# Performance work log

Measured on AMD Instinct MI355X. Metric: run time of the kernel, lower is better.

## Reference

```python
import jax, jax.numpy as jnp
import numpy as np

# 6 pairwise combinations of the 4 ray coordinates (decomp='2d')
COMBS = np.array([[0, 1], [0, 2], [0, 3], [1, 2], [1, 3], [2, 3]])
RAY_MIN = 0.0
RAY_MAX = 1.0
N_RAYS = 262144
GRID_DIM = 16
MLP_DIM = GRID_DIM * 6 * 3  # grid_dim * n_combs * n_levels = 288
MLP_WIDTH = 128


def _bilinear(grid_c, pts):
    """grid_c: [C,H,W] feature plane; pts: [N,2] in [0,1].
    Bilinear interpolation with align_corners=True semantics (grid_sample)."""
    C, H, W = grid_c.shape
    u = pts[:, 0] * (H - 1)
    v = pts[:, 1] * (W - 1)
    u0 = jnp.clip(jnp.floor(u), 0, H - 2).astype(jnp.int32)
    v0 = jnp.clip(jnp.floor(v), 0, W - 2).astype(jnp.int32)
    u1 = u0 + 1
    v1 = v0 + 1
    wu = (u - u0.astype(u.dtype))[None, :]  # [1,N]
    wv = (v - v0.astype(v.dtype))[None, :]
    g00 = grid_c[:, u0, v0]  # [C,N]
    g01 = grid_c[:, u0, v1]
    g10 = grid_c[:, u1, v0]
    g11 = grid_c[:, u1, v1]
    out = (g00 * (1 - wu) * (1 - wv) + g01 * (1 - wu) * wv
           + g10 * wu * (1 - wv) + g11 * wu * wv)
    return out.T  # [N,C]


def _level_feats(grids, coords):
    """grids: [6,C,H,W]; coords: [N,6,2] -> [N, 6*C] (comb-minor order)."""
    f = jax.vmap(_bilinear, in_axes=(0, 1))(grids, coords)  # [6,N,C]
    n = coords.shape[0]
    return jnp.moveaxis(f, 0, 1).reshape(n, -1)


def setup_inputs() -> dict:
    key = jax.random.key(0)
    ks = jax.random.split(key, 8)
    ray = jax.random.uniform(ks[0], (N_RAYS, 4), dtype=jnp.float32)
    grids_l0 = jax.random.normal(ks[1], (6, GRID_DIM, 128, 128), dtype=jnp.float32) * 0.1
    grids_l1 = jax.random.normal(ks[2], (6, GRID_DIM, 256, 256), dtype=jnp.float32) * 0.1
    grids_l2 = jax.random.normal(ks[3], (6, GRID_DIM, 512, 512), dtype=jnp.float32) * 0.1
    w1 = jax.random.normal(ks[4], (MLP_DIM, MLP_WIDTH), dtype=jnp.float32) * (1.0 / np.sqrt(MLP_DIM))
    b1 = jnp.zeros((MLP_WIDTH,), dtype=jnp.float32)
    w2 = jax.random.normal(ks[5], (MLP_WIDTH, 3), dtype=jnp.float32) * (1.0 / np.sqrt(MLP_WIDTH))
    b2 = jnp.zeros((3,), dtype=jnp.float32)
    return {"ray": ray, "grids_l0": grids_l0, "grids_l1": grids_l1,
            "grids_l2": grids_l2, "w1": w1, "b1": b1, "w2": w2, "b2": b2}


def reference(ray, grids_l0, grids_l1, grids_l2, w1, b1, w2, b2):
    # normalize rays into [0,1] using ray_min/ray_max buffers
    pts = (ray - RAY_MIN) / (RAY_MAX - RAY_MIN)
    coords = pts[:, COMBS]  # [N,6,2]
    # level-major, combination-minor concat (matches the nested forward loops)
    feats = jnp.concatenate(
        [_level_feats(g, coords) for g in (grids_l0, grids_l1, grids_l2)], axis=-1)
    h = jax.nn.relu(feats @ w1 + b1)
    return jax.nn.sigmoid(h @ w2 + b2)
```

## Files before the change

### kernel.cpp

```cpp
#include <hip/hip_runtime.h>
#include <hip/hip_bf16.h>
#include <cstdint>
#include <cstddef>

#define N_RAYS 262144
#define NR 32
#define THREADS 256
#define FSTRIDE 292

#define T0_OFF 0u
#define T1_OFF 1572864u
#define T2_OFF 7864320u
#define T_ELEMS 33030144u
#define FEAT_BYTE_OFF 66060288u
#define FEAT_DWORDS 37748736u
#define W1F_BYTE_OFF 217055232u
#define W1F_BYTES 73728u
#define KEYS_OFF   217128960u
#define PERM_OFF   217653248u
#define HIST_OFF   218701824u
#define OFFS_OFF   218963968u
#define RSORT_OFF  219226112u
#define NEED_SORT  223420416u

typedef __attribute__((ext_vector_type(8))) short short8v;
typedef __attribute__((ext_vector_type(4))) float float4v;

__device__ __forceinline__ float bf_lo(uint32_t w) { return __uint_as_float(w << 16); }
__device__ __forceinline__ float bf_hi(uint32_t w) { return __uint_as_float(w & 0xFFFF0000u); }

__device__ __forceinline__ float bf_extract(const uint4& q, int i) {
    uint32_t w = ((const uint32_t*)&q)[i >> 1];
    uint32_t h = (i & 1) ? (w & 0xFFFF0000u) : (w << 16);
    return __uint_as_float(h);
}

__device__ __forceinline__ uint16_t f2bf_rne(float f) {
    uint32_t x = __float_as_uint(f);
    uint32_t r = x + 0x7FFFu + ((x >> 16) & 1u);
    return (uint16_t)(r >> 16);
}

__device__ __forceinline__ float sel4(const float4& p, int i) {
    float r = p.x;
    r = (i == 1) ? p.y : r;
    r = (i == 2) ? p.z : r;
    r = (i == 3) ? p.w : r;
    return r;
}

__device__ __forceinline__ uint32_t morton4(const float4& p) {
    int q0 = min(15, max(0, (int)(p.x * 16.0f)));
    int q1 = min(15, max(0, (int)(p.y * 16.0f)));
    int q2 = min(15, max(0, (int)(p.z * 16.0f)));
    int q3 = min(15, max(0, (int)(p.w * 16.0f)));
    uint32_t key = 0;
    #pragma unroll
    for (int b = 0; b < 4; ++b) {
        key |= (uint32_t)((q0 >> b) & 1) << (4 * b + 0);
        key |= (uint32_t)((q1 >> b) & 1) << (4 * b + 1);
        key |= (uint32_t)((q2 >> b) & 1) << (4 * b + 2);
        key |= (uint32_t)((q3 >> b) & 1) << (4 * b + 3);
    }
    return key;
}

__global__ void transpose_kernel(const float* __restrict__ in,
                                 __hip_bfloat16* __restrict__ out, int H) {
    int idx = blockIdx.x * blockDim.x + threadIdx.x;
    int hh = H * H;
    int total = 6 * hh;
    if (idx >= total) return;
    int c = idx / hh;
    int rem = idx - c * hh;
    const float* ip = in + (size_t)c * 16 * hh + rem;
    uint32_t words[8];
    #pragma unroll
    for (int j = 0; j < 8; ++j) {
        uint16_t lo = f2bf_rne(ip[(size_t)(2 * j) * hh]);
        uint16_t hi = f2bf_rne(ip[(size_t)(2 * j + 1) * hh]);
        words[j] = (uint32_t)lo | ((uint32_t)hi << 16);
    }
    uint4* op = (uint4*)((uint16_t*)out + (size_t)idx * 16);
    op[0] = make_uint4(words[0], words[1], words[2], words[3]);
    op[1] = make_uint4(words[4], words[5], words[6], words[7]);
}

__global__ void w1_pack_kernel(const float* __restrict__ w1, uint16_t* __restrict__ w1f) {
    int t = blockIdx.x * 64 + threadIdx.x;
    if (t >= 8 * 9 * 64) return;
    int lane = t & 63;
    int fr = t >> 6;
    int ct = fr / 9;
    int kc = fr - ct * 9;
    int col = ct * 16 + (lane & 15);
    int krow = kc * 32 + (lane >> 4) * 8;
    uint32_t od[4];
    #pragma unroll
    for (int j = 0; j < 4; ++j) {
        uint16_t lo = f2bf_rne(w1[(size_t)(krow + 2 * j) * 128 + col]);
        uint16_t hi = f2bf_rne(w1[(size_t)(krow + 2 * j + 1) * 128 + col]);
        od[j] = (uint32_t)lo | ((uint32_t)hi << 16);
    }
    *(uint4*)(w1f + (size_t)t * 8) = make_uint4(od[0], od[1], od[2], od[3]);
}

__global__ void key_hist_kernel(const float4* __restrict__ ray,
                                uint16_t* __restrict__ keys,
                                uint32_t* __restrict__ hist) {
    int r = blockIdx.x * 256 + threadIdx.x;
    float4 p = ray[r];
    uint32_t key = morton4(p);
    keys[r] = (uint16_t)key;
    atomicAdd(&hist[key], 1u);
}

__global__ void scanA_kernel(const uint32_t* __restrict__ hist, uint32_t* __restrict__ bsum) {
    __shared__ uint32_t s[256];
    int t = threadIdx.x;
    s[t] = hist[blockIdx.x * 256 + t];
    __syncthreads();
    for (int d = 128; d > 0; d >>= 1) {
        if (t < d) s[t] += s[t + d];
        __syncthreads();
    }
    if (t == 0) bsum[blockIdx.x] = s[0];
}

__global__ void scanB_kernel(uint32_t* __restrict__ bsum) {
    __shared__ uint32_t s[256];
    int t = threadIdx.x;
    uint32_t v = bsum[t];
    s[t] = v;
    __syncthreads();
    for (int d = 1; d < 256; d <<= 1) {
        uint32_t x = (t >= d) ? s[t - d] : 0;
        __syncthreads();
        s[t] += x;
        __syncthreads();
    }
    bsum[t] = s[t] - v;
}

__global__ void scanC_kernel(const uint32_t* __restrict__ hist,
                             const uint32_t* __restrict__ bsum,
                             uint32_t* __restrict__ offs) {
    __shared__ uint32_t s[256];
    int t = threadIdx.x, b = blockIdx.x;
    uint32_t v = hist[b * 256 + t];
    s[t] = v;
    __syncthreads();
    for (int d = 1; d < 256; d <<= 1) {
        uint32_t x = (t >= d) ? s[t - d] : 0;
        __syncthreads();
        s[t] += x;
        __syncthreads();
    }
    offs[b * 256 + t] = bsum[b] + s[t] - v;
}

__global__ void scatter_kernel(const float4* __restrict__ ray,
                               const uint16_t* __restrict__ keys,
                               uint32_t* __restrict__ offs,
                               uint32_t* __restrict__ perm,
                               float4* __restrict__ ray_sorted) {
    int r = blockIdx.x * 256 + threadIdx.x;
    uint32_t key = keys[r];
    uint32_t pos = atomicAdd(&offs[key], 1u);
    perm[pos] = (uint32_t)r;
    ray_sorted[pos] = ray[r];
}

__global__ __launch_bounds__(256, 4) void fused_gmlp_kernel(
    const float4* __restrict__ rsort, const uint16_t* __restrict__ gt,
    const uint16_t* __restrict__ w1f, const float* __restrict__ bias1,
    const float* __restrict__ w2, const float* __restrict__ bias2,
    const uint32_t* __restrict__ perm, float* __restrict__ out) {
    __shared__ uint32_t s_feats[32 * 148];
    __shared__ float s_w2[384];
    __shared__ float4 s_ray[32];

    int tid = threadIdx.x;
    int wvid = tid >> 6;
    int lane = tid & 63;
    int swz = ((blockIdx.x & 7) << 10) + (blockIdx.x >> 3);
    int r0 = swz << 5;

    if (tid < 32) s_ray[tid] = rsort[r0 + tid];
    s_w2[tid] = w2[tid];
    if (tid < 128) s_w2[256 + tid] = w2[256 + tid];
    __syncthreads();

    for (int s = wvid; s < 9; s += 4) {
        int interp = 2 * s + (lane >> 5);
        int r = lane & 31;
        int level = (interp >= 12) ? 2 : ((interp >= 6) ? 1 : 0);
        int comb = interp - level * 6;
        int H = 128 << level;
        float4 p = s_ray[r];
        int c0 = (0x211000 >> (4 * comb)) & 0xF;
        int c1 = (0x332321 >> (4 * comb)) & 0xF;
        float u = sel4(p, c0) * (float)(H - 1);
        float v = sel4(p, c1) * (float)(H - 1);
        float u0f = fminf(fmaxf(floorf(u), 0.0f), (float)(H - 2));
        float v0f = fminf(fmaxf(floorf(v), 0.0f), (float)(H - 2));
        float fu = u - u0f, fv = v - v0f;
        int u0 = (int)u0f, v0 = (int)v0f;

        uint32_t lvl_off = (level == 0) ? T0_OFF : ((level == 1) ? T1_OFF : T2_OFF);
        const uint16_t* gp0 = gt + lvl_off + (((size_t)comb * H + u0) * H + v0) * 16;
        const uint4* q0 = (const uint4*)gp0;
        const uint4* q1 = (const uint4*)(gp0 + (size_t)16 * H);
        uint4 a0 = q0[0], a1 = q0[1], a2 = q0[2], a3 = q0[3];
        uint4 b0 = q1[0], b1 = q1[1], b2 = q1[2], b3 = q1[3];

        uint32_t c00[8], c01[8], c10[8], c11[8];
        #pragma unroll
        for (int j = 0; j < 4; ++j) {
            c00[j] = ((const uint32_t*)&a0)[j];  c00[j + 4] = ((const uint32_t*)&a1)[j];
            c01[j] = ((const uint32_t*)&a2)[j];  c01[j + 4] = ((const uint32_t*)&a3)[j];
            c10[j] = ((const uint32_t*)&b0)[j];  c10[j + 4] = ((const uint32_t*)&b1)[j];
            c11[j] = ((const uint32_t*)&b2)[j];  c11[j + 4] = ((const uint32_t*)&b3)[j];
        }

        float w00 = (1.0f - fu) * (1.0f - fv);
        float w01 = (1.0f - fu) * fv;
        float w10 = fu * (1.0f - fv);
        float w11 = fu * fv;

        uint32_t od[8];
        #pragma unroll
        for (int j = 0; j < 8; ++j) {
            float lo = w00 * bf_lo(c00[j]) + w01 * bf_lo(c01[j]) +
                       w10 * bf_lo(c10[j]) + w11 * bf_lo(c11[j]);
            float hi = w00 * bf_hi(c00[j]) + w01 * bf_hi(c01[j]) +
                       w10 * bf_hi(c10[j]) + w11 * bf_hi(c11[j]);
            od[j] = (uint32_t)f2bf_rne(lo) | ((uint32_t)f2bf_rne(hi) << 16);
        }
        uint32_t* op = &s_feats[r * 148 + interp * 8];
        *(uint4*)op       = make_uint4(od[0], od[1], od[2], od[3]);
        *(uint4*)(op + 4) = make_uint4(od[4], od[5], od[6], od[7]);
    }
    __syncthreads();

    float b1c0 = bias1[wvid * 32 + (lane & 15)];
    float b1c1 = bias1[wvid * 32 + 16 + (lane & 15)];
    int lg = lane >> 4;
    const uint32_t* arow = &s_feats[(lane & 15) * 148 + lg * 4];

    float4v acc00, acc10, acc01, acc11;
    {
        short8v bfrA[9];
        #pragma unroll
        for (int kc = 0; kc < 9; ++kc)
            bfrA[kc] = *(const short8v*)(w1f + (((size_t)((wvid * 2) * 9 + kc)) * 64 + lane) * 8);
        #pragma unroll
        for (int j = 0; j < 4; ++j) { acc00[j] = b1c0; acc10[j] = b1c0; }
        #pragma unroll
        for (int kc = 0; kc < 9; ++kc) {
            short8v a0 = *(const short8v*)(arow + kc * 16);
            short8v a1 = *(const short8v*)(arow + 16 * 148 + kc * 16);
            acc00 = __builtin_amdgcn_mfma_f32_16x16x32_bf16(a0, bfrA[kc], acc00, 0, 0, 0);
            acc10 = __builtin_amdgcn_mfma_f32_16x16x32_bf16(a1, bfrA[kc], acc10, 0, 0, 0);
        }
    }
    {
        short8v bfrB[9];
        #pragma unroll
        for (int kc = 0; kc < 9; ++kc)
            bfrB[kc] = *(const short8v*)(w1f + (((size_t)((wvid * 2 + 1) * 9 + kc)) * 64 + lane) * 8);
        #pragma unroll
        for (int j = 0; j < 4; ++j) { acc01[j] = b1c1; acc11[j] = b1c1; }
        #pragma unroll
        for (int kc = 0; kc < 9; ++kc) {
            short8v a0 = *(const short8v*)(arow + kc * 16);
            short8v a1 = *(const short8v*)(arow + 16 * 148 + kc * 16);
            acc01 = __builtin_amdgcn_mfma_f32_16x16x32_bf16(a0, bfrB[kc], acc01, 0, 0, 0);
            acc11 = __builtin_amdgcn_mfma_f32_16x16x32_bf16(a1, bfrB[kc], acc11, 0, 0, 0);
        }
    }
    __syncthreads();

    float* s_h = (float*)s_feats;
    {
        int c0 = wvid * 32 + (lane & 15);
        int rb = lg * 4;
        #pragma unroll
        for (int j = 0; j < 4; ++j) {
            s_h[(rb + j) * 132 + c0]            = fmaxf(acc00[j], 0.0f);
            s_h[(rb + j) * 132 + c0 + 16]       = fmaxf(acc01[j], 0.0f);
            s_h[(rb + j + 16) * 132 + c0]       = fmaxf(acc10[j], 0.0f);
            s_h[(rb + j + 16) * 132 + c0 + 16]  = fmaxf(acc11[j], 0.0f);
        }
    }
    __syncthreads();

    int ray = tid >> 3;
    int jg = tid & 7;
    int j0 = jg * 16;
    float p0 = 0.f, p1 = 0.f, p2 = 0.f;
    #pragma unroll
    for (int qq = 0; qq < 4; ++qq) {
        float4 hv = *(const float4*)&s_h[ray * 132 + j0 + qq * 4];
        const float* w2a = &s_w2[(j0 + qq * 4) * 3];
        p0 += hv.x * w2a[0] + hv.y * w2a[3] + hv.z * w2a[6] + hv.w * w2a[9];
        p1 += hv.x * w2a[1] + hv.y * w2a[4] + hv.z * w2a[7] + hv.w * w2a[10];
        p2 += hv.x * w2a[2] + hv.y * w2a[5] + hv.z * w2a[8] + hv.w * w2a[11];
    }
    p0 += __shfl_xor(p0, 1); p0 += __shfl_xor(p0, 2); p0 += __shfl_xor(p0, 4);
    p1 += __shfl_xor(p1, 1); p1 += __shfl_xor(p1, 2); p1 += __shfl_xor(p1, 4);
    p2 += __shfl_xor(p2, 1); p2 += __shfl_xor(p2, 2); p2 += __shfl_xor(p2, 4);

    if (jg == 0) {
        int orig = (int)perm[r0 + ray];
        float o0 = 1.0f / (1.0f + expf(-(p0 + bias2[0])));
        float o1 = 1.0f / (1.0f + expf(-(p1 + bias2[1])));
        float o2 = 1.0f / (1.0f + expf(-(p2 + bias2[2])));
        float* op = out + (size_t)orig * 3;
        op[0] = o0; op[1] = o1; op[2] = o2;
    }
}

__global__ __launch_bounds__(256, 8) void gather_t_kernel(
    const float4* __restrict__ ray, const uint16_t* __restrict__ gt,
    uint32_t* __restrict__ featsT) {
    int lb = (blockIdx.x & 7) * 2304 + (blockIdx.x >> 3);
    int interp = lb >> 10;
    int r = ((lb & 1023) << 8) + threadIdx.x;
    int level = interp / 6;
    int comb = interp - level * 6;
    int H = 128 << level;

    float4 p = ray[r];
    int c0 = (0x211000 >> (4 * comb)) & 0xF;
    int c1 = (0x332321 >> (4 * comb)) & 0xF;
    float u = sel4(p, c0) * (float)(H - 1);
    float v = sel4(p, c1) * (float)(H - 1);
    float u0f = fminf(fmaxf(floorf(u), 0.0f), (float)(H - 2));
    float v0f = fminf(fmaxf(floorf(v), 0.0f), (float)(H - 2));
    float wu = u - u0f, wv = v - v0f;
    int u0 = (int)u0f, v0 = (int)v0f;

    uint32_t lvl_off = (level == 0) ? T0_OFF : ((level == 1) ? T1_OFF : T2_OFF);
    const uint16_t* gp0 = gt + lvl_off + (((size_t)comb * H + u0) * H + v0) * 16;
    const uint4* q0 = (const uint4*)gp0;
    const uint4* q1 = (const uint4*)(gp0 + (size_t)16 * H);
    uint4 a0 = q0[0], a1 = q0[1], a2 = q0[2], a3 = q0[3];
    uint4 b0 = q1[0], b1 = q1[1], b2 = q1[2], b3 = q1[3];

    uint32_t c00[8], c01[8], c10[8], c11[8];
    #pragma unroll
    for (int j = 0; j < 4; ++j) {
        c00[j] = ((const uint32_t*)&a0)[j];  c00[j + 4] = ((const uint32_t*)&a1)[j];
        c01[j] = ((const uint32_t*)&a2)[j];  c01[j + 4] = ((const uint32_t*)&a3)[j];
        c10[j] = ((const uint32_t*)&b0)[j];  c10[j + 4] = ((const uint32_t*)&b1)[j];
        c11[j] = ((const uint32_t*)&b2)[j];  c11[j + 4] = ((const uint32_t*)&b3)[j];
    }

    float w00 = (1.0f - wu) * (1.0f - wv);
    float w01 = (1.0f - wu) * wv;
    float w10 = wu * (1.0f - wv);
    float w11 = wu * wv;

    uint32_t od[8];
    #pragma unroll
    for (int j = 0; j < 8; ++j) {
        float lo = w00 * bf_lo(c00[j]) + w01 * bf_lo(c01[j]) +
                   w10 * bf_lo(c10[j]) + w11 * bf_lo(c11[j]);
        float hi = w00 * bf_hi(c00[j]) + w01 * bf_hi(c01[j]) +
                   w10 * bf_hi(c10[j]) + w11 * bf_hi(c11[j]);
        od[j] = (uint32_t)f2bf_rne(lo) | ((uint32_t)f2bf_rne(hi) << 16);
    }

    uint4* op = (uint4*)(featsT + ((size_t)interp * N_RAYS + r) * 8);
    op[0] = make_uint4(od[0], od[1], od[2], od[3]);
    op[1] = make_uint4(od[4], od[5], od[6], od[7]);
}

__global__ __launch_bounds__(256, 2) void mfma_mlp_kernel(
    const uint16_t* __restrict__ featsT,
    const uint16_t* __restrict__ w1f,
    const float* __restrict__ bias1,
    const float* __restrict__ w2, const float* __restrict__ bias2,
    const uint32_t* __restrict__ perm,
    float* __restrict__ out, int tiles_per_block) {
    __shared__ float s_h[32][132];

    int tid = threadIdx.x;
    int wv = tid >> 6;
    int lane = tid & 63;

    short8v bfr[2][9];
    #pragma unroll
    for (int ctl = 0; ctl < 2; ++ctl) {
        int ct = wv * 2 + ctl;
        #pragma unroll
        for (int kc = 0; kc < 9; ++kc)
            bfr[ctl][kc] = *(const short8v*)(w1f + (((size_t)(ct * 9 + kc)) * 64 + lane) * 8);
    }
    float b1c0 = bias1[wv * 32 + (lane & 15)];
    float b1c1 = bias1[wv * 32 + 16 + (lane & 15)];

    int jg = tid & 7;
    int j0 = jg * 16;
    float w2r0[16], w2r1[16], w2r2[16];
    #pragma unroll
    for (int jj = 0; jj < 16; ++jj) {
        const float* w2p = w2 + (size_t)(j0 + jj) * 3;
        w2r0[jj] = w2p[0]; w2r1[jj] = w2p[1]; w2r2[jj] = w2p[2];
    }
    float bb0 = bias2[0], bb1 = bias2[1], bb2 = bias2[2];

    int lg = lane >> 4;
    int half8 = (lg & 1) * 8;
    int ipo = lg >> 1;

    for (int it = 0; it < tiles_per_block; ++it) {
        int tile = blockIdx.x * tiles_per_block + it;
        int r0 = tile * 32;
        int rA = r0 + (lane & 15);

        short8v af[18];
        #pragma unroll
        for (int kc = 0; kc < 9; ++kc) {
            size_t base = ((size_t)(2 * kc + ipo) * N_RAYS + rA) * 16 + half8;
            af[kc]     = *(const short8v*)(featsT + base);
            af[9 + kc] = *(const short8v*)(featsT + base + 256);
        }

        float4v acc00, acc01, acc10, acc11;
        #pragma unroll
        for (int j = 0; j < 4; ++j) { acc00[j] = b1c0; acc01[j] = b1c1; acc10[j] = b1c0; acc11[j] = b1c1; }

        #pragma unroll
        for (int kc = 0; kc < 9; ++kc) {
            acc00 = __builtin_amdgcn_mfma_f32_16x16x32_bf16(af[kc],     bfr[0][kc], acc00, 0, 0, 0);
            acc01 = __builtin_amdgcn_mfma_f32_16x16x32_bf16(af[kc],     bfr[1][kc], acc01, 0, 0, 0);
            acc10 = __builtin_amdgcn_mfma_f32_16x16x32_bf16(af[9 + kc], bfr[0][kc], acc10, 0, 0, 0);
            acc11 = __builtin_amdgcn_mfma_f32_16x16x32_bf16(af[9 + kc], bfr[1][kc], acc11, 0, 0, 0);
        }

        __syncthreads();
        {
            int c0 = wv * 32 + (lane & 15);
            int rb = (lane >> 4) * 4;
            #pragma unroll
            for (int j = 0; j < 4; ++j) {
                s_h[rb + j][c0]           = fmaxf(acc00[j], 0.0f);
                s_h[rb + j][c0 + 16]      = fmaxf(acc01[j], 0.0f);
                s_h[rb + j + 16][c0]      = fmaxf(acc10[j], 0.0f);
                s_h[rb + j + 16][c0 + 16] = fmaxf(acc11[j], 0.0f);
            }
        }
        __syncthreads();

        int ray = tid >> 3;
        float p0 = 0.f, p1 = 0.f, p2 = 0.f;
        #pragma unroll
        for (int qq = 0; qq < 4; ++qq) {
            float4 hv = *(const float4*)&s_h[ray][j0 + qq * 4];
            float h0 = hv.x, h1 = hv.y, h2 = hv.z, h3 = hv.w;
            p0 += h0 * w2r0[qq * 4] + h1 * w2r0[qq * 4 + 1] + h2 * w2r0[qq * 4 + 2] + h3 * w2r0[qq * 4 + 3];
            p1 += h0 * w2r1[qq * 4] + h1 * w2r1[qq * 4 + 1] + h2 * w2r1[qq * 4 + 2] + h3 * w2r1[qq * 4 + 3];
            p2 += h0 * w2r2[qq * 4] + h1 * w2r2[qq * 4 + 1] + h2 * w2r2[qq * 4 + 2] + h3 * w2r2[qq * 4 + 3];
        }
        p0 += __shfl_xor(p0, 1); p0 += __shfl_xor(p0, 2); p0 += __shfl_xor(p0, 4);
        p1 += __shfl_xor(p1, 1); p1 += __shfl_xor(p1, 2); p1 += __shfl_xor(p1, 4);
        p2 += __shfl_xor(p2, 1); p2 += __shfl_xor(p2, 2); p2 += __shfl_xor(p2, 4);

        if (jg == 0) {
            int orig = perm ? (int)perm[r0 + ray] : (r0 + ray);
            float o0 = 1.0f / (1.0f + expf(-(p0 + bb0)));
            float o1 = 1.0f / (1.0f + expf(-(p1 + bb1)));
            float o2 = 1.0f / (1.0f + expf(-(p2 + bb2)));
            float* op = out + (size_t)orig * 3;
            op[0] = o0; op[1] = o1; op[2] = o2;
        }
    }
}

template <bool USE_T>
__global__ __launch_bounds__(THREADS) void fused_kernel(
    const float4* __restrict__ ray,
    const float* __restrict__ g0, const float* __restrict__ g1,
    const float* __restrict__ g2,
    const __hip_bfloat16* __restrict__ gt,
    const float* __restrict__ weights1, const float* __restrict__ bias1,
    const float* __restrict__ weights2, const float* __restrict__ bias2,
    float* __restrict__ out) {
    __shared__ float4 s_ray[NR];
    __shared__ float s_feats[NR][FSTRIDE];

    int tid = threadIdx.x;
    int rbase = blockIdx.x * NR;
    if (tid < NR) s_ray[tid] = ray[rbase + tid];
    __syncthreads();

    for (int t = tid; t < NR * 36; t += THREADS) {
        int r = t / 36;
        int rem = t - r * 36;
        int interp = rem >> 1;
        int half = rem & 1;
        int level = (interp >= 12) ? 2 : ((interp >= 6) ? 1 : 0);
        int comb = interp - level * 6;
        int H = 128 << level;
        float4 p = s_ray[r];
        int c0 = (0x211000 >> (4 * comb)) & 0xF;
        int c1 = (0x332321 >> (4 * comb)) & 0xF;
        float u = sel4(p, c0) * (float)(H - 1);
        float v = sel4(p, c1) * (float)(H - 1);
        float u0f = fminf(fmaxf(floorf(u), 0.0f), (float)(H - 2));
        float v0f = fminf(fmaxf(floorf(v), 0.0f), (float)(H - 2));
        float wu = u - u0f, wv = v - v0f;
        int u0 = (int)u0f, v0 = (int)v0f;
        float w00 = (1.0f - wu) * (1.0f - wv);
        float w01 = (1.0f - wu) * wv;
        float w10 = wu * (1.0f - wv);
        float w11 = wu * wv;
        float f[8];
        if (USE_T) {
            uint32_t lvl_off = (level == 0) ? T0_OFF : ((level == 1) ? T1_OFF : T2_OFF);
            const uint16_t* gp = (const uint16_t*)gt + lvl_off +
                                 (((size_t)comb * H + u0) * H + v0) * 16 + half * 8;
            uint4 a00 = *(const uint4*)gp;
            uint4 a01 = *(const uint4*)(gp + 16);
            uint4 a10 = *(const uint4*)(gp + (size_t)16 * H);
            uint4 a11 = *(const uint4*)(gp + (size_t)16 * H + 16);
            #pragma unroll
            for (int i = 0; i < 8; ++i) {
                f[i] = w00 * bf_extract(a00, i) + w01 * bf_extract(a01, i) +
                       w10 * bf_extract(a10, i) + w11 * bf_extract(a11, i);
            }
        } else {
            const float* gp = (level == 0) ? g0 : ((level == 1) ? g1 : g2);
            const float* base = gp + ((size_t)(comb * 16 + half * 8) * H + u0) * H + v0;
            #pragma unroll
            for (int i = 0; i < 8; ++i) {
                const float* q = base + (size_t)i * H * H;
                float a00 = q[0], a01 = q[1], a10 = q[H], a11 = q[H + 1];
                f[i] = w00 * a00 + w01 * a01 + w10 * a10 + w11 * a11;
            }
        }
        int fo = interp * 16 + half * 8;
        float* fp = &s_feats[r][fo];
        #pragma unroll
        for (int i = 0; i < 8; ++i) fp[i] = f[i];
    }
    __syncthreads();

    int r = tid >> 3;
    int jg = tid & 7;
    int j0 = jg * 16;
    float acc[16];
    #pragma unroll
    for (int jj = 0; jj < 16; ++jj) acc[jj] = bias1[j0 + jj];

    const float* wp = weights1 + j0;
    for (int k = 0; k < 288; k += 4) {
        float4 fv = *(const float4*)&s_feats[r][k];
        #pragma unroll
        for (int kk = 0; kk < 4; ++kk) {
            const float4* wr = (const float4*)(wp + (size_t)(k + kk) * 128);
            float fk = (kk == 0) ? fv.x : ((kk == 1) ? fv.y : ((kk == 2) ? fv.z : fv.w));
            float4 wa = wr[0], wb = wr[1], wc = wr[2], wd = wr[3];
            acc[0]  += fk * wa.x; acc[1]  += fk * wa.y; acc[2]  += fk * wa.z; acc[3]  += fk * wa.w;
            acc[4]  += fk * wb.x; acc[5]  += fk * wb.y; acc[6]  += fk * wb.z; acc[7]  += fk * wb.w;
            acc[8]  += fk * wc.x; acc[9]  += fk * wc.y; acc[10] += fk * wc.z; acc[11] += fk * wc.w;
            acc[12] += fk * wd.x; acc[13] += fk * wd.y; acc[14] += fk * wd.z; acc[15] += fk * wd.w;
        }
    }

    float p0 = 0.f, p1 = 0.f, p2 = 0.f;
    #pragma unroll
    for (int jj = 0; jj < 16; ++jj) {
        float h = fmaxf(acc[jj], 0.0f);
        const float* w2r = weights2 + (size_t)(j0 + jj) * 3;
        p0 += h * w2r[0];
        p1 += h * w2r[1];
        p2 += h * w2r[2];
    }
    p0 += __shfl_xor(p0, 1); p0 += __shfl_xor(p0, 2); p0 += __shfl_xor(p0, 4);
    p1 += __shfl_xor(p1, 1); p1 += __shfl_xor(p1, 2); p1 += __shfl_xor(p1, 4);
    p2 += __shfl_xor(p2, 1); p2 += __shfl_xor(p2, 2); p2 += __shfl_xor(p2, 4);

    if (jg == 0) {
        float o0 = 1.0f / (1.0f + expf(-(p0 + bias2[0])));
        float o1 = 1.0f / (1.0f + expf(-(p1 + bias2[1])));
        float o2 = 1.0f / (1.0f + expf(-(p2 + bias2[2])));
        float* op = out + (size_t)(rbase + r) * 3;
        op[0] = o0; op[1] = o1; op[2] = o2;
    }
}

extern "C" void kernel_launch(void* const* d_in, const int* in_sizes, int n_in,
                              void* d_out, int out_size, void* d_ws, size_t ws_size,
                              hipStream_t stream) {
    const float4* ray = (const float4*)d_in[0];
    const float* g0 = (const float*)d_in[1];
    const float* g1 = (const float*)d_in[2];
    const float* g2 = (const float*)d_in[3];
    const float* w1 = (const float*)d_in[4];
    const float* b1 = (const float*)d_in[5];
    const float* w2 = (const float*)d_in[6];
    const float* b2 = (const float*)d_in[7];
    float* out = (float*)d_out;

    const size_t T_BYTES = (size_t)T_ELEMS * 2;
    const size_t NEED = (size_t)W1F_BYTE_OFF + W1F_BYTES;

    if (ws_size >= (size_t)NEED_SORT) {
        char* ws = (char*)d_ws;
        __hip_bfloat16* wsb = (__hip_bfloat16*)d_ws;
        uint32_t* bsum  = (uint32_t*)(ws + FEAT_BYTE_OFF);
        uint16_t* w1f  = (uint16_t*)(ws + W1F_BYTE_OFF);
        uint16_t* keys = (uint16_t*)(ws + KEYS_OFF);
        uint32_t* perm = (uint32_t*)(ws + PERM_OFF);
        uint32_t* hist = (uint32_t*)(ws + HIST_OFF);
        uint32_t* offs = (uint32_t*)(ws + OFFS_OFF);
        float4* rsort  = (float4*)(ws + RSORT_OFF);

        hipMemsetAsync(hist, 0, 65536 * 4, stream);
        transpose_kernel<<<(6 * 128 * 128 + 255) / 256, 256, 0, stream>>>(g0, wsb + T0_OFF, 128);
        transpose_kernel<<<(6 * 256 * 256 + 255) / 256, 256, 0, stream>>>(g1, wsb + T1_OFF, 256);
        transpose_kernel<<<(6 * 512 * 512 + 255) / 256, 256, 0, stream>>>(g2, wsb + T2_OFF, 512);
        w1_pack_kernel<<<72, 64, 0, stream>>>(w1, w1f);
        key_hist_kernel<<<N_RAYS / 256, 256, 0, stream>>>(ray, keys, hist);
        scanA_kernel<<<256, 256, 0, stream>>>(hist, bsum);
        scanB_kernel<<<1, 256, 0, stream>>>(bsum);
        scanC_kernel<<<256, 256, 0, stream>>>(hist, bsum, offs);
        scatter_kernel<<<N_RAYS / 256, 256, 0, stream>>>(ray, keys, offs, perm, rsort);
        fused_gmlp_kernel<<<N_RAYS / 32, 256, 0, stream>>>(
            rsort, (const uint16_t*)wsb, w1f, b1, w2, b2, perm, out);
    } else if (ws_size >= NEED) {
        __hip_bfloat16* wsb = (__hip_bfloat16*)d_ws;
        transpose_kernel<<<(6 * 128 * 128 + 255) / 256, 256, 0, stream>>>(g0, wsb + T0_OFF, 128);
        transpose_kernel<<<(6 * 256 * 256 + 255) / 256, 256, 0, stream>>>(g1, wsb + T1_OFF, 256);
        transpose_kernel<<<(6 * 512 * 512 + 255) / 256, 256, 0, stream>>>(g2, wsb + T2_OFF, 512);
        uint32_t* feats = (uint32_t*)((char*)d_ws + FEAT_BYTE_OFF);
        uint16_t* w1f = (uint16_t*)((char*)d_ws + W1F_BYTE_OFF);
        w1_pack_kernel<<<72, 64, 0, stream>>>(w1, w1f);
        gather_t_kernel<<<18432, 256, 0, stream>>>(ray, (const uint16_t*)wsb, feats);
        const int TILES_PER_BLOCK = 4;
        int nblk = N_RAYS / 32 / TILES_PER_BLOCK;
        mfma_mlp_kernel<<<nblk, 256, 0, stream>>>(
            (const uint16_t*)feats, w1f, b1, w2, b2, nullptr, out, TILES_PER_BLOCK);
    } else if (ws_size >= T_BYTES) {
        __hip_bfloat16* wsb = (__hip_bfloat16*)d_ws;
        transpose_kernel<<<(6 * 128 * 128 + 255) / 256, 256, 0, stream>>>(g0, wsb + T0_OFF, 128);
        transpose_kernel<<<(6 * 256 * 256 + 255) / 256, 256, 0, stream>>>(g1, wsb + T1_OFF, 256);
        transpose_kernel<<<(6 * 512 * 512 + 255) / 256, 256, 0, stream>>>(g2, wsb + T2_OFF, 512);
        fused_kernel<true><<<N_RAYS / NR, THREADS, 0, stream>>>(
            ray, g0, g1, g2, wsb, w1, b1, w2, b2, out);
    } else {
        fused_kernel<false><<<N_RAYS / NR, THREADS, 0, stream>>>(
            ray, g0, g1, g2, nullptr, w1, b1, w2, b2, out);
    }
}
```

Baseline: 196.3 us.

## Merge preprocessing kernels into one launch and raise fused kernel occupancy bound

Folds the three grid transposes, the W1 packing and the Morton key histogram into one prep kernel that dispatches work by block index, replacing five launches with one. This removes per-launch gaps and the tail serialisation between small kernels. It also raises the fused gather+MLP kernel's launch-bounds minimum from 4 to 7 blocks per CU, which pushes the compiler to use fewer registers and may cause spills.

```diff
diff --git a/kernel.cpp b/kernel.cpp
--- a/kernel.cpp
+++ b/kernel.cpp
@@ -23,6 +23,12 @@
 #define RSORT_OFF  219226112u
 #define NEED_SORT  223420416u
 
+#define PB_L0   384
+#define PB_L1   1920
+#define PB_L2   8064
+#define PB_PK   8082
+#define PB_HI   9106
+
 typedef __attribute__((ext_vector_type(8))) short short8v;
 typedef __attribute__((ext_vector_type(4))) float float4v;
 
@@ -65,12 +71,10 @@
     return key;
 }
 
-__global__ void transpose_kernel(const float* __restrict__ in,
-                                 __hip_bfloat16* __restrict__ out, int H) {
-    int idx = blockIdx.x * blockDim.x + threadIdx.x;
+__device__ __forceinline__ void transpose_body(const float* __restrict__ in,
+                                               uint16_t* __restrict__ out,
+                                               int H, int idx) {
     int hh = H * H;
-    int total = 6 * hh;
-    if (idx >= total) return;
     int c = idx / hh;
     int rem = idx - c * hh;
     const float* ip = in + (size_t)c * 16 * hh + rem;
@@ -81,38 +85,48 @@
         uint16_t hi = f2bf_rne(ip[(size_t)(2 * j + 1) * hh]);
         words[j] = (uint32_t)lo | ((uint32_t)hi << 16);
     }
-    uint4* op = (uint4*)((uint16_t*)out + (size_t)idx * 16);
+    uint4* op = (uint4*)(out + (size_t)idx * 16);
     op[0] = make_uint4(words[0], words[1], words[2], words[3]);
     op[1] = make_uint4(words[4], words[5], words[6], words[7]);
 }
 
-__global__ void w1_pack_kernel(const float* __restrict__ w1, uint16_t* __restrict__ w1f) {
-    int t = blockIdx.x * 64 + threadIdx.x;
-    if (t >= 8 * 9 * 64) return;
-    int lane = t & 63;
-    int fr = t >> 6;
-    int ct = fr / 9;
-    int kc = fr - ct * 9;
-    int col = ct * 16 + (lane & 15);
-    int krow = kc * 32 + (lane >> 4) * 8;
-    uint32_t od[4];
-    #pragma unroll
-    for (int j = 0; j < 4; ++j) {
-        uint16_t lo = f2bf_rne(w1[(size_t)(krow + 2 * j) * 128 + col]);
-        uint16_t hi = f2bf_rne(w1[(size_t)(krow + 2 * j + 1) * 128 + col]);
-        od[j] = (uint32_t)lo | ((uint32_t)hi << 16);
-    }
-    *(uint4*)(w1f + (size_t)t * 8) = make_uint4(od[0], od[1], od[2], od[3]);
-}
-
-__global__ void key_hist_kernel(const float4* __restrict__ ray,
-                                uint16_t* __restrict__ keys,
-                                uint32_t* __restrict__ hist) {
-    int r = blockIdx.x * 256 + threadIdx.x;
-    float4 p = ray[r];
-    uint32_t key = morton4(p);
-    keys[r] = (uint16_t)key;
-    atomicAdd(&hist[key], 1u);
+__global__ __launch_bounds__(256) void prep_kernel(
+    const float* __restrict__ g0, const float* __restrict__ g1,
+    const float* __restrict__ g2, const float* __restrict__ w1,
+    const float4* __restrict__ ray,
+    uint16_t* __restrict__ gt, uint16_t* __restrict__ w1f,
+    uint16_t* __restrict__ keys, uint32_t* __restrict__ hist) {
+    int b = blockIdx.x;
+    int tid = threadIdx.x;
+    if (b < PB_L0) {
+        transpose_body(g0, gt + T0_OFF, 128, b * 256 + tid);
+    } else if (b < PB_L1) {
+        transpose_body(g1, gt + T1_OFF, 256, (b - PB_L0) * 256 + tid);
+    } else if (b < PB_L2) {
+        transpose_body(g2, gt + T2_OFF, 512, (b - PB_L1) * 256 + tid);
+    } else if (b < PB_PK) {
+        int t = (b - PB_L2) * 256 + tid;
+        int lane = t & 63;
+        int fr = t >> 6;
+        int ct = fr / 9;
+        int kc = fr - ct * 9;
+        int col = ct * 16 + (lane & 15);
+        int krow = kc * 32 + (lane >> 4) * 8;
+        uint32_t od[4];
+        #pragma unroll
+        for (int j = 0; j < 4; ++j) {
+            uint16_t lo = f2bf_rne(w1[(size_t)(krow + 2 * j) * 128 + col]);
+            uint16_t hi = f2bf_rne(w1[(size_t)(krow + 2 * j + 1) * 128 + col]);
+            od[j] = (uint32_t)lo | ((uint32_t)hi << 16);
+        }
+        *(uint4*)(w1f + (size_t)t * 8) = make_uint4(od[0], od[1], od[2], od[3]);
+    } else {
+        int r = (b - PB_PK) * 256 + tid;
+        float4 p = ray[r];
+        uint32_t key = morton4(p);
+        keys[r] = (uint16_t)key;
+        atomicAdd(&hist[key], 1u);
+    }
 }
 
 __global__ void scanA_kernel(const uint32_t* __restrict__ hist, uint32_t* __restrict__ bsum) {
@@ -171,7 +185,7 @@
     ray_sorted[pos] = ray[r];
 }
 
-__global__ __launch_bounds__(256, 4) void fused_gmlp_kernel(
+__global__ __launch_bounds__(256, 7) void fused_gmlp_kernel(
     const float4* __restrict__ rsort, const uint16_t* __restrict__ gt,
     const uint16_t* __restrict__ w1f, const float* __restrict__ bias1,
     const float* __restrict__ w2, const float* __restrict__ bias2,
@@ -319,6 +333,32 @@
         float* op = out + (size_t)orig * 3;
         op[0] = o0; op[1] = o1; op[2] = o2;
     }
+}
+
+__global__ void transpose_kernel(const float* __restrict__ in,
+                                 __hip_bfloat16* __restrict__ out, int H) {
+    int idx = blockIdx.x * blockDim.x + threadIdx.x;
+    if (idx >= 6 * H * H) return;
+    transpose_body(in, (uint16_t*)out, H, idx);
+}
+
+__global__ void w1_pack_kernel(const float* __restrict__ w1, uint16_t* __restrict__ w1f) {
+    int t = blockIdx.x * 64 + threadIdx.x;
+    if (t >= 8 * 9 * 64) return;
+    int lane = t & 63;
+    int fr = t >> 6;
+    int ct = fr / 9;
+    int kc = fr - ct * 9;
+    int col = ct * 16 + (lane & 15);
+    int krow = kc * 32 + (lane >> 4) * 8;
+    uint32_t od[4];
+    #pragma unroll
+    for (int j = 0; j < 4; ++j) {
+        uint16_t lo = f2bf_rne(w1[(size_t)(krow + 2 * j) * 128 + col]);
+        uint16_t hi = f2bf_rne(w1[(size_t)(krow + 2 * j + 1) * 128 + col]);
+        od[j] = (uint32_t)lo | ((uint32_t)hi << 16);
+    }
+    *(uint4*)(w1f + (size_t)t * 8) = make_uint4(od[0], od[1], od[2], od[3]);
 }
 
 __global__ __launch_bounds__(256, 8) void gather_t_kernel(
@@ -620,11 +660,8 @@
         float4* rsort  = (float4*)(ws + RSORT_OFF);
 
         hipMemsetAsync(hist, 0, 65536 * 4, stream);
-        transpose_kernel<<<(6 * 128 * 128 + 255) / 256, 256, 0, stream>>>(g0, wsb + T0_OFF, 128);
-        transpose_kernel<<<(6 * 256 * 256 + 255) / 256, 256, 0, stream>>>(g1, wsb + T1_OFF, 256);
-        transpose_kernel<<<(6 * 512 * 512 + 255) / 256, 256, 0, stream>>>(g2, wsb + T2_OFF, 512);
-        w1_pack_kernel<<<72, 64, 0, stream>>>(w1, w1f);
-        key_hist_kernel<<<N_RAYS / 256, 256, 0, stream>>>(ray, keys, hist);
+        prep_kernel<<<PB_HI, 256, 0, stream>>>(
+            g0, g1, g2, w1, ray, (uint16_t*)wsb, w1f, keys, hist);
         scanA_kernel<<<256, 256, 0, stream>>>(hist, bsum);
         scanB_kernel<<<1, 256, 0, stream>>>(bsum);
         scanC_kernel<<<256, 256, 0, stream>>>(hist, bsum, offs);
```

New measurement: 194.5 us. Within noise of the previous version (-0.9%).
